# Performance work log

Hardware: AMD Instinct MI355X
Metric: run time of the kernel (lower is better)

The kernel has to match this reference:

```python
import jax, jax.numpy as jnp
import numpy as np

DFAUD = 1024
DFRGB = 1024
DIM_K = 1024
N_HEADS = 4
B, T = 16, 1024


def setup_inputs() -> dict:
    key = jax.random.key(0)
    ks = jax.random.split(key, 11)
    s = lambda d: 1.0 / np.sqrt(d)
    return {
        "x": jax.random.normal(ks[0], (B, T, DFAUD), jnp.float32),
        "y": jax.random.normal(ks[1], (B, T, DFRGB), jnp.float32),
        "adj": jax.random.normal(ks[2], (B, T, T), jnp.float32),
        "Wq": jax.random.uniform(ks[3], (DIM_K, DFAUD), jnp.float32, -s(DFAUD), s(DFAUD)),
        "bq": jnp.zeros((DIM_K,), jnp.float32),
        "Wk": jax.random.uniform(ks[4], (DIM_K, DFRGB), jnp.float32, -s(DFRGB), s(DFRGB)),
        "bk": jnp.zeros((DIM_K,), jnp.float32),
        "Wv": jax.random.uniform(ks[5], (DIM_K, DFRGB), jnp.float32, -s(DFRGB), s(DFRGB)),
        "bv": jnp.zeros((DIM_K,), jnp.float32),
        "Wo": jax.random.uniform(ks[6], (DFRGB, DIM_K), jnp.float32, -s(DIM_K), s(DIM_K)),
        "bo": jnp.zeros((DFRGB,), jnp.float32),
    }


def reference(x, y, adj, Wq, bq, Wk, bk, Wv, bv, Wo, bo):
    b, t = x.shape[0], x.shape[1]
    dh = DIM_K // N_HEADS
    norm = 1.0 / np.sqrt(DIM_K)
    # Faithful reproduction of the torch reshape(-1, B, T, dim_k // n_heads):
    # [B, T, dim_k] -> [n_heads, B, T, dh] (row-major reshape, layout-mixing for h>1)
    Q = (x @ Wq.T + bq).reshape(N_HEADS, b, t, dh)
    K = (y @ Wk.T + bk).reshape(N_HEADS, b, t, dh)
    V = (y @ Wv.T + bv).reshape(N_HEADS, b, t, dh)
    scores = jnp.einsum('hbqd,hbkd->hbqk', Q, K) * norm  # [h, B, T, T]
    att = jax.nn.softmax(scores + adj, axis=-1)          # adj [B,T,T] broadcasts
    temp = jnp.einsum('hbqk,hbkd->hbqd', att, V).reshape(b, t, DIM_K)
    out = (temp @ Wo.T + bo).reshape(-1, t, y.shape[2])
    return out
```

## Files before the change

### kernel.cpp

```cpp
#include <hip/hip_runtime.h>
#include <stdint.h>
#include <string.h>

typedef unsigned short u16;
typedef __attribute__((ext_vector_type(8))) short short8_t;
typedef __attribute__((ext_vector_type(4))) float f32x4;

typedef const __attribute__((address_space(1))) void GV;
typedef __attribute__((address_space(3))) void LV;

__device__ __forceinline__ void gload_lds16(const void* g, void* l) {
  __builtin_amdgcn_global_load_lds((GV*)g, (LV*)l, 16, 0, 0);
}

__device__ __forceinline__ u16 f2bf(float f) {
  union { float f; uint32_t u; } v; v.f = f;
  return (u16)((v.u + 0x7FFFu + ((v.u >> 16) & 1u)) >> 16);
}

__device__ __forceinline__ f32x4 fz4() { f32x4 v = {0.f, 0.f, 0.f, 0.f}; return v; }

__global__ __launch_bounds__(256) void cast2_kernel(const float* __restrict__ in0,
                                                    const float* __restrict__ in1,
                                                    u16* __restrict__ out0,
                                                    u16* __restrict__ out1) {
  const int half = blockIdx.x >> 14;
  const float* in = half ? in1 : in0;
  u16* out = half ? out1 : out0;
  int i = ((blockIdx.x & 16383) * 256 + threadIdx.x) * 4;
  float4 v = *(const float4*)(in + i);
  ushort4 o;
  o.x = f2bf(v.x); o.y = f2bf(v.y); o.z = f2bf(v.z); o.w = f2bf(v.w);
  *(ushort4*)(out + i) = o;
}

__global__ __launch_bounds__(256) void cast4_kernel(const float* __restrict__ w0,
                                                    const float* __restrict__ w1,
                                                    const float* __restrict__ w2,
                                                    const float* __restrict__ w3,
                                                    u16* __restrict__ o0,
                                                    u16* __restrict__ o1,
                                                    u16* __restrict__ o2,
                                                    u16* __restrict__ o3) {
  const int sel = blockIdx.x >> 10;
  const float* in = sel == 0 ? w0 : sel == 1 ? w1 : sel == 2 ? w2 : w3;
  u16* out = sel == 0 ? o0 : sel == 1 ? o1 : sel == 2 ? o2 : o3;
  int i = ((blockIdx.x & 1023) * 256 + threadIdx.x) * 4;
  float4 v = *(const float4*)(in + i);
  ushort4 o;
  o.x = f2bf(v.x); o.y = f2bf(v.y); o.z = f2bf(v.z); o.w = f2bf(v.w);
  *(ushort4*)(out + i) = o;
}

template <int OUT_BF16>
__global__ __launch_bounds__(512, 2) void gemm8(const u16* __restrict__ A,
                                                const u16* __restrict__ B,
                                                const float* __restrict__ bias,
                                                void* __restrict__ Cout,
                                                int M, int N, int K) {
  __shared__ u16 Al[2 * 16384];
  __shared__ u16 Bl[2 * 16384];
  const int tid = threadIdx.x, w = tid >> 6, l = tid & 63;
  const int g = l >> 4, q = l & 15;
  const int bid = blockIdx.x;
  const int xcd = bid & 7;
  const int nt = (bid >> 3) & 3;
  const int mt = xcd * 8 + (bid >> 5);
  const int n0 = nt * 256, m0 = mt * 256;
  const int wr = (w >> 2) * 128, wc = (w & 3) * 64;
  const int NT = K >> 6;
  const int ah = w >> 2;
  const int bh = (w & 3) >> 1;
  const int brow0 = ((w & 3) & 1) * 64;

#define STAGE_A(S, half)                                                          \
  {                                                                               \
    _Pragma("unroll") for (int j_ = 0; j_ < 2; ++j_) {                            \
      const int idx_ = j_ * 512 + tid;                                            \
      const int row_ = idx_ >> 3;                                                 \
      const int sl_ = (idx_ & 7) ^ (((idx_ >> 5) & 1) << 1);                      \
      gload_lds16(A + (size_t)(m0 + (half) * 128 + row_) * K + (S) * 64 + sl_ * 8,\
                  Al + ((S) & 1) * 16384 + (half) * 8192 + (j_ * 512 + w * 64) * 8);\
    }                                                                             \
  }
#define STAGE_B(S, half)                                                          \
  {                                                                               \
    _Pragma("unroll") for (int j_ = 0; j_ < 2; ++j_) {                            \
      const int idx_ = j_ * 512 + tid;                                            \
      const int row_ = idx_ >> 3;                                                 \
      const int sl_ = (idx_ & 7) ^ (((idx_ >> 5) & 1) << 1);                      \
      gload_lds16(B + (size_t)(n0 + (half) * 128 + row_) * K + (S) * 64 + sl_ * 8,\
                  Bl + ((S) & 1) * 16384 + (half) * 8192 + (j_ * 512 + w * 64) * 8);\
    }                                                                             \
  }

  f32x4 acc[8][4];
#pragma unroll
  for (int i = 0; i < 8; ++i)
#pragma unroll
    for (int n = 0; n < 4; ++n) acc[i][n] = fz4();

  float bv[4];
#pragma unroll
  for (int nf = 0; nf < 4; ++nf) bv[nf] = bias[n0 + wc + nf * 16 + q];

  STAGE_A(0, 0); STAGE_A(0, 1); STAGE_B(0, 0); STAGE_B(0, 1);
  STAGE_A(1, 0); STAGE_A(1, 1); STAGE_B(1, 0); STAGE_B(1, 1);
  asm volatile("s_waitcnt vmcnt(8)");
  __builtin_amdgcn_s_barrier();

  short8_t bfr[4][2];
  for (int S = 0; S < NT; ++S) {
    const int bs = (S & 1) * 16384;
#pragma unroll
    for (int p = 0; p < 4; ++p) {
      short8_t afr[2][2];
#pragma unroll
      for (int mi = 0; mi < 2; ++mi)
#pragma unroll
        for (int kk = 0; kk < 2; ++kk) {
          const int r = (2 * p + mi) * 16 + q;
          afr[mi][kk] = *(const short8_t*)(Al + bs + ah * 8192 + r * 64 +
                                           ((kk * 4 + g) ^ (((r >> 2) & 1) << 1)) * 8);
        }
      if (p == 0) {
#pragma unroll
        for (int nf = 0; nf < 4; ++nf)
#pragma unroll
          for (int kk = 0; kk < 2; ++kk) {
            const int r = brow0 + nf * 16 + q;
            bfr[nf][kk] = *(const short8_t*)(Bl + bs + bh * 8192 + r * 64 +
                                             ((kk * 4 + g) ^ (((r >> 2) & 1) << 1)) * 8);
          }
      }
      if (p == 0 && S >= 1 && S + 1 < NT) STAGE_A(S + 1, 0);
      if (p == 1 && S >= 1 && S + 1 < NT) STAGE_A(S + 1, 1);
      if (p == 2 && S + 2 < NT) STAGE_B(S + 2, 0);
      if (p == 3 && S + 2 < NT) STAGE_B(S + 2, 1);
      if (p == 3) {
        if (S == NT - 2) { asm volatile("s_waitcnt vmcnt(0)"); }
        else if (S < NT - 2) { asm volatile("s_waitcnt vmcnt(4)"); }
      }
      __builtin_amdgcn_s_barrier();
      asm volatile("s_waitcnt lgkmcnt(0)" ::: "memory");
      __builtin_amdgcn_sched_barrier(0);
      __builtin_amdgcn_s_setprio(1);
#pragma unroll
      for (int nf = 0; nf < 4; ++nf)
#pragma unroll
        for (int mi = 0; mi < 2; ++mi)
#pragma unroll
          for (int kk = 0; kk < 2; ++kk)
            acc[2 * p + mi][nf] = __builtin_amdgcn_mfma_f32_16x16x32_bf16(
                afr[mi][kk], bfr[nf][kk], acc[2 * p + mi][nf], 0, 0, 0);
      __builtin_amdgcn_s_setprio(0);
      __builtin_amdgcn_s_barrier();
    }
  }
#undef STAGE_A
#undef STAGE_B

#pragma unroll
  for (int nf = 0; nf < 4; ++nf) {
    const int col = n0 + wc + nf * 16 + q;
#pragma unroll
    for (int mf = 0; mf < 8; ++mf) {
      const int rowb = m0 + wr + mf * 16 + g * 4;
#pragma unroll
      for (int j = 0; j < 4; ++j) {
        const float vv = acc[mf][nf][j] + bv[nf];
        if (OUT_BF16)
          ((u16*)Cout)[(size_t)(rowb + j) * N + col] = f2bf(vv);
        else
          ((float*)Cout)[(size_t)(rowb + j) * N + col] = vv;
      }
    }
  }
}

__global__ __launch_bounds__(256) void transpose_v(const u16* __restrict__ V,
                                                   u16* __restrict__ VT) {
  __shared__ u16 t[64][68];
  const int hb = blockIdx.z;
  const int t0 = blockIdx.x * 64, d0 = blockIdx.y * 64;
  const u16* src = V + (size_t)hb * 1024 * 256;
  u16* dst = VT + (size_t)hb * 256 * 1024;
  const int tid = threadIdx.x;
#pragma unroll
  for (int i = 0; i < 4; ++i) {
    const int idx = i * 256 + tid;
    const int r = idx >> 4, c4 = (idx & 15) * 4;
    ushort4 v = *(const ushort4*)(src + (size_t)(t0 + r) * 256 + d0 + c4);
    *(ushort4*)&t[r][c4] = v;
  }
  __syncthreads();
#pragma unroll
  for (int i = 0; i < 4; ++i) {
    const int idx = i * 256 + tid;
    const int r = idx >> 4, c4 = (idx & 15) * 4;
    ushort4 v;
    v.x = t[c4][r]; v.y = t[c4 + 1][r]; v.z = t[c4 + 2][r]; v.w = t[c4 + 3][r];
    *(ushort4*)(dst + (size_t)(d0 + r) * 1024 + t0 + c4) = v;
  }
}

__global__ __launch_bounds__(256) void attn_kernel(const u16* __restrict__ Q,
                                                   const u16* __restrict__ Kf,
                                                   const u16* __restrict__ VT,
                                                   const float* __restrict__ adj,
                                                   u16* __restrict__ O) {
  __shared__ u16 Ks[32 * 256];
  __shared__ u16 Vs[256 * 32];
  const int tid = threadIdx.x, w = tid >> 6, l = tid & 63;
  const int g = l >> 4, q = l & 15;
  const int bid = blockIdx.x;
  const int xcd = bid & 7, idx = bid >> 3;
  const int b = xcd * 2 + (idx >> 6);
  const int qb = (idx >> 2) & 15, h = idx & 3;
  const int hb = h * 16 + b;
  const int q0 = qb * 64;
  const u16* qb_p = Q + ((size_t)hb * 1024 + q0 + w * 16) * 256;
  const u16* kb = Kf + (size_t)hb * 1024 * 256;
  const u16* vtb = VT + (size_t)hb * 256 * 1024;
  const float* adjr = adj + (size_t)b * 1024 * 1024 + (size_t)(q0 + w * 16 + q) * 1024;

  const int krow_b = tid >> 5;
  const int kslot = tid & 31;
  const int vdr_b = tid >> 2;
  const int vsl = tid & 3;

  short8_t qf[8];
#pragma unroll
  for (int kk = 0; kk < 8; ++kk)
    qf[kk] = *(const short8_t*)(qb_p + (size_t)q * 256 + kk * 32 + g * 8);

  f32x4 o[16];
#pragma unroll
  for (int n = 0; n < 16; ++n) o[n] = fz4();
  float mrun = -1e30f, lrun = 0.f;

  short8_t kst[4], vst[4];

#define LOADREGS(ktt)                                                              \
  {                                                                                \
    _Pragma("unroll") for (int i_ = 0; i_ < 4; ++i_) {                             \
      const int row_ = i_ * 8 + krow_b;                                            \
      kst[i_] = *(const short8_t*)(kb + (size_t)((ktt) * 32 + row_) * 256 +        \
                                   kslot * 8);                                     \
    }                                                                              \
    _Pragma("unroll") for (int i_ = 0; i_ < 4; ++i_) {                             \
      const int dr_ = i_ * 64 + vdr_b;                                             \
      vst[i_] = *(const short8_t*)(vtb + (size_t)dr_ * 1024 + (ktt) * 32 +         \
                                   vsl * 8);                                       \
    }                                                                              \
  }
#define WRITEREGS()                                                                \
  {                                                                                \
    _Pragma("unroll") for (int i_ = 0; i_ < 4; ++i_) {                             \
      const int row_ = i_ * 8 + krow_b;                                            \
      *(short8_t*)((char*)Ks + row_ * 512 + ((kslot ^ (row_ & 7)) * 16)) = kst[i_];\
    }                                                                              \
    _Pragma("unroll") for (int i_ = 0; i_ < 4; ++i_) {                             \
      const int dr_ = i_ * 64 + vdr_b;                                             \
      *(short8_t*)((char*)Vs + dr_ * 64 + ((vsl ^ ((dr_ >> 1) & 3)) * 16)) = vst[i_];\
    }                                                                              \
  }

  LOADREGS(0);
  float4 a0 = *(const float4*)(adjr + 0 * 32 + 0 * 16 + g * 4);
  float4 a1 = *(const float4*)(adjr + 0 * 32 + 1 * 16 + g * 4);
  WRITEREGS();
  __syncthreads();

  for (int kt = 0; kt < 32; ++kt) {
    float4 n0v = a0, n1v = a1;
    if (kt < 31) {
      LOADREGS(kt + 1);
      n0v = *(const float4*)(adjr + (kt + 1) * 32 + 0 * 16 + g * 4);
      n1v = *(const float4*)(adjr + (kt + 1) * 32 + 1 * 16 + g * 4);
    }

    f32x4 s[2];
    __builtin_amdgcn_s_setprio(1);
#pragma unroll
    for (int f = 0; f < 2; ++f) {
      f32x4 a = fz4();
      const int row = f * 16 + q;
      const char* kr = (const char*)Ks + row * 512;
#pragma unroll
      for (int kk = 0; kk < 8; ++kk) {
        const int cb = kk * 64 + g * 16;
        short8_t kfr = *(const short8_t*)(kr + (cb ^ ((row & 7) << 4)));
        a = __builtin_amdgcn_mfma_f32_16x16x32_bf16(kfr, qf[kk], a, 0, 0, 0);
      }
      s[f] = a;
    }
    __builtin_amdgcn_s_setprio(0);

#pragma unroll
    for (int j = 0; j < 4; ++j) {
      s[0][j] = s[0][j] * 0.03125f + ((const float*)&a0)[j];
      s[1][j] = s[1][j] * 0.03125f + ((const float*)&a1)[j];
    }

    float pmax = s[0][0];
#pragma unroll
    for (int j = 1; j < 4; ++j) pmax = fmaxf(pmax, s[0][j]);
#pragma unroll
    for (int j = 0; j < 4; ++j) pmax = fmaxf(pmax, s[1][j]);
    pmax = fmaxf(pmax, __shfl_xor(pmax, 16));
    pmax = fmaxf(pmax, __shfl_xor(pmax, 32));

    if (!__all(pmax - mrun <= 8.0f)) {
      const float mn = fmaxf(mrun, pmax);
      const float al = __expf(mrun - mn);
      mrun = mn;
      lrun *= al;
#pragma unroll
      for (int n = 0; n < 16; ++n)
#pragma unroll
        for (int r = 0; r < 4; ++r) o[n][r] *= al;
    }

    float sum = 0.f;
#pragma unroll
    for (int f = 0; f < 2; ++f)
#pragma unroll
      for (int j = 0; j < 4; ++j) {
        const float p = __expf(s[f][j] - mrun);
        s[f][j] = p;
        sum += p;
      }
    sum += __shfl_xor(sum, 16);
    sum += __shfl_xor(sum, 32);
    lrun += sum;

    uint32_t W00, W01, W10, W11;
    asm("v_cvt_pk_bf16_f32 %0, %1, %2" : "=v"(W00) : "v"(s[0][0]), "v"(s[0][1]));
    asm("v_cvt_pk_bf16_f32 %0, %1, %2" : "=v"(W01) : "v"(s[0][2]), "v"(s[0][3]));
    asm("v_cvt_pk_bf16_f32 %0, %1, %2" : "=v"(W10) : "v"(s[1][0]), "v"(s[1][1]));
    asm("v_cvt_pk_bf16_f32 %0, %1, %2" : "=v"(W11) : "v"(s[1][2]), "v"(s[1][3]));
    const uint32_t sA0 = (g < 2) ? W00 : W10;
    const uint32_t sA1 = (g < 2) ? W01 : W11;
    const uint32_t sB0 = (g < 2) ? W10 : W00;
    const uint32_t sB1 = (g < 2) ? W11 : W01;
    const uint32_t A0 = (uint32_t)__shfl_xor((int)sA0, 16);
    const uint32_t A1 = (uint32_t)__shfl_xor((int)sA1, 16);
    const uint32_t B0 = (uint32_t)__shfl_xor((int)sB0, 32);
    const uint32_t B1 = (uint32_t)__shfl_xor((int)sB1, 32);
    const uint32_t C0 = (uint32_t)__shfl_xor((int)sB0, 48);
    const uint32_t C1 = (uint32_t)__shfl_xor((int)sB1, 48);
    union { uint32_t u[4]; short8_t v; } pu;
    pu.u[0] = (g == 0) ? W00 : (g == 1) ? C0 : (g == 2) ? B0 : A0;
    pu.u[1] = (g == 0) ? W01 : (g == 1) ? C1 : (g == 2) ? B1 : A1;
    pu.u[2] = (g == 0) ? A0 : (g == 1) ? B0 : (g == 2) ? C0 : W10;
    pu.u[3] = (g == 0) ? A1 : (g == 1) ? B1 : (g == 2) ? C1 : W11;
    const short8_t pa = pu.v;

    __builtin_amdgcn_s_setprio(1);
#pragma unroll
    for (int n = 0; n < 16; ++n) {
      const int dr = n * 16 + q;
      const int sl = g ^ ((dr >> 1) & 3);
      short8_t vf = *(const short8_t*)((const char*)Vs + dr * 64 + sl * 16);
      o[n] = __builtin_amdgcn_mfma_f32_16x16x32_bf16(vf, pa, o[n], 0, 0, 0);
    }
    __builtin_amdgcn_s_setprio(0);

    if (kt < 31) {
      __syncthreads();
      WRITEREGS();
      __syncthreads();
    }
    a0 = n0v; a1 = n1v;
  }
#undef LOADREGS
#undef WRITEREGS

  const float inv = 1.0f / lrun;
  u16* ob = O + ((size_t)hb * 1024 + q0 + w * 16 + q) * 256;
#pragma unroll
  for (int n = 0; n < 16; ++n) {
    ushort4 st;
    st.x = f2bf(o[n][0] * inv); st.y = f2bf(o[n][1] * inv);
    st.z = f2bf(o[n][2] * inv); st.w = f2bf(o[n][3] * inv);
    *(ushort4*)(ob + n * 16 + g * 4) = st;
  }
}

extern "C" void kernel_launch(void* const* d_in, const int* in_sizes, int n_in,
                              void* d_out, int out_size, void* d_ws, size_t ws_size,
                              hipStream_t stream) {
  (void)in_sizes; (void)n_in; (void)out_size; (void)ws_size;
  const float* x   = (const float*)d_in[0];
  const float* y   = (const float*)d_in[1];
  const float* adj = (const float*)d_in[2];
  const float* Wq  = (const float*)d_in[3];
  const float* bq  = (const float*)d_in[4];
  const float* Wk  = (const float*)d_in[5];
  const float* bk  = (const float*)d_in[6];
  const float* Wv  = (const float*)d_in[7];
  const float* bv  = (const float*)d_in[8];
  const float* Wo  = (const float*)d_in[9];
  const float* bo  = (const float*)d_in[10];

  char* ws = (char*)d_ws;
  const size_t MB = 1ull << 20;
  u16* Xb  = (u16*)(ws + 0);
  u16* Yb  = (u16*)(ws + 32 * MB);
  u16* Wqb = (u16*)(ws + 64 * MB);
  u16* Wkb = (u16*)(ws + 66 * MB);
  u16* Wvb = (u16*)(ws + 68 * MB);
  u16* Wob = (u16*)(ws + 70 * MB);
  u16* Qb  = (u16*)(ws + 72 * MB);
  u16* Kb  = (u16*)(ws + 104 * MB);
  u16* Vb  = (u16*)(ws + 136 * MB);
  u16* VTb = (u16*)(ws + 168 * MB);
  u16* Tmp = Xb;

  cast2_kernel<<<32768, 256, 0, stream>>>(x, y, Xb, Yb);
  cast4_kernel<<<4096, 256, 0, stream>>>(Wq, Wk, Wv, Wo, Wqb, Wkb, Wvb, Wob);

  gemm8<1><<<256, 512, 0, stream>>>(Xb, Wqb, bq, Qb, 16384, 1024, 1024);
  gemm8<1><<<256, 512, 0, stream>>>(Yb, Wkb, bk, Kb, 16384, 1024, 1024);
  gemm8<1><<<256, 512, 0, stream>>>(Yb, Wvb, bv, Vb, 16384, 1024, 1024);

  transpose_v<<<dim3(16, 4, 64), 256, 0, stream>>>(Vb, VTb);

  attn_kernel<<<1024, 256, 0, stream>>>(Qb, Kb, VTb, adj, Tmp);

  gemm8<0><<<256, 512, 0, stream>>>(Tmp, Wob, bo, d_out, 16384, 1024, 1024);
}
```

Before: 356.5 us.

## Fuse QKV projections into one launch and write V pre-transposed from epilogue

Merges the three Q/K/V projection GEMMs into a single 768-block launch that selects operands by block index, and has the V GEMM epilogue write directly into the transposed per-head layout the attention kernel expects. This removes the separate transpose kernel, its extra read and write of V, and two launch gaps, while giving the GPU three times as many blocks to schedule. The transposed epilogue scatters 2-byte stores with a large stride, which may coalesce poorly.

```diff
diff --git a/kernel.cpp b/kernel.cpp
--- a/kernel.cpp
+++ b/kernel.cpp
@@ -52,22 +52,19 @@
   *(ushort4*)(out + i) = o;
 }
 
-template <int OUT_BF16>
-__global__ __launch_bounds__(512, 2) void gemm8(const u16* __restrict__ A,
-                                                const u16* __restrict__ B,
-                                                const float* __restrict__ bias,
-                                                void* __restrict__ Cout,
-                                                int M, int N, int K) {
-  __shared__ u16 Al[2 * 16384];
-  __shared__ u16 Bl[2 * 16384];
+__device__ __forceinline__ void gemm8_core(int bid, const u16* __restrict__ A,
+                                           const u16* __restrict__ B,
+                                           const float* __restrict__ bias,
+                                           void* __restrict__ Cout, int mode,
+                                           u16* Al, u16* Bl) {
+  const int M = 16384, N = 1024, K = 1024;
+  (void)M;
   const int tid = threadIdx.x, w = tid >> 6, l = tid & 63;
   const int g = l >> 4, q = l & 15;
-  const int bid = blockIdx.x;
   const int xcd = bid & 7;
   const int nt = (bid >> 3) & 3;
   const int mt = xcd * 8 + (bid >> 5);
   const int n0 = nt * 256, m0 = mt * 256;
-  const int wr = (w >> 2) * 128, wc = (w & 3) * 64;
   const int NT = K >> 6;
   const int ah = w >> 2;
   const int bh = (w & 3) >> 1;
@@ -102,7 +99,7 @@
 
   float bv[4];
 #pragma unroll
-  for (int nf = 0; nf < 4; ++nf) bv[nf] = bias[n0 + wc + nf * 16 + q];
+  for (int nf = 0; nf < 4; ++nf) bv[nf] = bias[n0 + (w & 3) * 64 + nf * 16 + q];
 
   STAGE_A(0, 0); STAGE_A(0, 1); STAGE_B(0, 0); STAGE_B(0, 1);
   STAGE_A(1, 0); STAGE_A(1, 1); STAGE_B(1, 0); STAGE_B(1, 1);
@@ -160,6 +157,7 @@
 #undef STAGE_A
 #undef STAGE_B
 
+  const int wr = (w >> 2) * 128, wc = (w & 3) * 64;
 #pragma unroll
   for (int nf = 0; nf < 4; ++nf) {
     const int col = n0 + wc + nf * 16 + q;
@@ -169,39 +167,52 @@
 #pragma unroll
       for (int j = 0; j < 4; ++j) {
         const float vv = acc[mf][nf][j] + bv[nf];
-        if (OUT_BF16)
-          ((u16*)Cout)[(size_t)(rowb + j) * N + col] = f2bf(vv);
-        else
-          ((float*)Cout)[(size_t)(rowb + j) * N + col] = vv;
+        const int row = rowb + j;
+        if (mode == 0) {
+          ((float*)Cout)[(size_t)row * N + col] = vv;
+        } else if (mode == 1) {
+          ((u16*)Cout)[(size_t)row * N + col] = f2bf(vv);
+        } else {
+          ((u16*)Cout)[((size_t)(row >> 8) << 18) + ((size_t)(col & 255) << 10) +
+                       ((row & 255) * 4) + (col >> 8)] = f2bf(vv);
+        }
       }
     }
   }
 }
 
-__global__ __launch_bounds__(256) void transpose_v(const u16* __restrict__ V,
-                                                   u16* __restrict__ VT) {
-  __shared__ u16 t[64][68];
-  const int hb = blockIdx.z;
-  const int t0 = blockIdx.x * 64, d0 = blockIdx.y * 64;
-  const u16* src = V + (size_t)hb * 1024 * 256;
-  u16* dst = VT + (size_t)hb * 256 * 1024;
-  const int tid = threadIdx.x;
-#pragma unroll
-  for (int i = 0; i < 4; ++i) {
-    const int idx = i * 256 + tid;
-    const int r = idx >> 4, c4 = (idx & 15) * 4;
-    ushort4 v = *(const ushort4*)(src + (size_t)(t0 + r) * 256 + d0 + c4);
-    *(ushort4*)&t[r][c4] = v;
-  }
-  __syncthreads();
-#pragma unroll
-  for (int i = 0; i < 4; ++i) {
-    const int idx = i * 256 + tid;
-    const int r = idx >> 4, c4 = (idx & 15) * 4;
-    ushort4 v;
-    v.x = t[c4][r]; v.y = t[c4 + 1][r]; v.z = t[c4 + 2][r]; v.w = t[c4 + 3][r];
-    *(ushort4*)(dst + (size_t)(d0 + r) * 1024 + t0 + c4) = v;
-  }
+__global__ __launch_bounds__(512, 2) void gemm8_qkv(const u16* __restrict__ Xb,
+                                                    const u16* __restrict__ Yb,
+                                                    const u16* __restrict__ Wqb,
+                                                    const u16* __restrict__ Wkb,
+                                                    const u16* __restrict__ Wvb,
+                                                    const float* __restrict__ bq,
+                                                    const float* __restrict__ bk,
+                                                    const float* __restrict__ bv,
+                                                    u16* __restrict__ Qb,
+                                                    u16* __restrict__ Kb,
+                                                    u16* __restrict__ VTb) {
+  __shared__ u16 Al[2 * 16384];
+  __shared__ u16 Bl[2 * 16384];
+  const int sel = blockIdx.x >> 8, bid = blockIdx.x & 255;
+  const u16* A;
+  const u16* B;
+  const float* bias;
+  void* C;
+  int mode;
+  if (sel == 0)      { A = Xb; B = Wqb; bias = bq; C = Qb;  mode = 1; }
+  else if (sel == 1) { A = Yb; B = Wkb; bias = bk; C = Kb;  mode = 1; }
+  else               { A = Yb; B = Wvb; bias = bv; C = VTb; mode = 2; }
+  gemm8_core(bid, A, B, bias, C, mode, Al, Bl);
+}
+
+__global__ __launch_bounds__(512, 2) void gemm8_out(const u16* __restrict__ A,
+                                                    const u16* __restrict__ B,
+                                                    const float* __restrict__ bias,
+                                                    float* __restrict__ C) {
+  __shared__ u16 Al[2 * 16384];
+  __shared__ u16 Bl[2 * 16384];
+  gemm8_core(blockIdx.x, A, B, bias, C, 0, Al, Bl);
 }
 
 __global__ __launch_bounds__(256) void attn_kernel(const u16* __restrict__ Q,
@@ -414,20 +425,15 @@
   u16* Wob = (u16*)(ws + 70 * MB);
   u16* Qb  = (u16*)(ws + 72 * MB);
   u16* Kb  = (u16*)(ws + 104 * MB);
-  u16* Vb  = (u16*)(ws + 136 * MB);
   u16* VTb = (u16*)(ws + 168 * MB);
   u16* Tmp = Xb;
 
   cast2_kernel<<<32768, 256, 0, stream>>>(x, y, Xb, Yb);
   cast4_kernel<<<4096, 256, 0, stream>>>(Wq, Wk, Wv, Wo, Wqb, Wkb, Wvb, Wob);
 
-  gemm8<1><<<256, 512, 0, stream>>>(Xb, Wqb, bq, Qb, 16384, 1024, 1024);
-  gemm8<1><<<256, 512, 0, stream>>>(Yb, Wkb, bk, Kb, 16384, 1024, 1024);
-  gemm8<1><<<256, 512, 0, stream>>>(Yb, Wvb, bv, Vb, 16384, 1024, 1024);
-
-  transpose_v<<<dim3(16, 4, 64), 256, 0, stream>>>(Vb, VTb);
+  gemm8_qkv<<<768, 512, 0, stream>>>(Xb, Yb, Wqb, Wkb, Wvb, bq, bk, bv, Qb, Kb, VTb);
 
   attn_kernel<<<1024, 256, 0, stream>>>(Qb, Kb, VTb, adj, Tmp);
 
-  gemm8<0><<<256, 512, 0, stream>>>(Tmp, Wob, bo, d_out, 16384, 1024, 1024);
-}
+  gemm8_out<<<256, 512, 0, stream>>>(Tmp, Wob, bo, (float*)d_out);
+}
```

After: 380.0 us. +6.6%, slower.

## Fuse V transpose into V projection GEMM epilogue with permuted B rows

Applied to the files above, without the earlier changes.

Adds a third GEMM mode that loads the V weight rows in a permuted order and writes its output straight into the transposed V layout the attention kernel expects. The separate transpose kernel and the intermediate V buffer go away, which removes one launch and a full 32MB read and write pass. The cost is a scattered epilogue store pattern, with 2-byte writes strided by 1024 elements, which may coalesce poorly.

```diff
diff --git a/kernel.cpp b/kernel.cpp
--- a/kernel.cpp
+++ b/kernel.cpp
@@ -52,7 +52,7 @@
   *(ushort4*)(out + i) = o;
 }
 
-template <int OUT_BF16>
+template <int MODE>
 __global__ __launch_bounds__(512, 2) void gemm8(const u16* __restrict__ A,
                                                 const u16* __restrict__ B,
                                                 const float* __restrict__ bias,
@@ -67,11 +67,12 @@
   const int nt = (bid >> 3) & 3;
   const int mt = xcd * 8 + (bid >> 5);
   const int n0 = nt * 256, m0 = mt * 256;
-  const int wr = (w >> 2) * 128, wc = (w & 3) * 64;
   const int NT = K >> 6;
   const int ah = w >> 2;
   const int bh = (w & 3) >> 1;
   const int brow0 = ((w & 3) & 1) * 64;
+
+#define BROW(u) (MODE == 2 ? ((((u) >> 6) << 8) + nt * 64 + ((u) & 63)) : (n0 + (u)))
 
 #define STAGE_A(S, half)                                                          \
   {                                                                               \
@@ -89,7 +90,8 @@
       const int idx_ = j_ * 512 + tid;                                            \
       const int row_ = idx_ >> 3;                                                 \
       const int sl_ = (idx_ & 7) ^ (((idx_ >> 5) & 1) << 1);                      \
-      gload_lds16(B + (size_t)(n0 + (half) * 128 + row_) * K + (S) * 64 + sl_ * 8,\
+      const int pr_ = BROW((half) * 128 + row_);                                  \
+      gload_lds16(B + (size_t)pr_ * K + (S) * 64 + sl_ * 8,                       \
                   Bl + ((S) & 1) * 16384 + (half) * 8192 + (j_ * 512 + w * 64) * 8);\
     }                                                                             \
   }
@@ -100,9 +102,10 @@
 #pragma unroll
     for (int n = 0; n < 4; ++n) acc[i][n] = fz4();
 
+  const int wc = (w & 3) * 64;
   float bv[4];
 #pragma unroll
-  for (int nf = 0; nf < 4; ++nf) bv[nf] = bias[n0 + wc + nf * 16 + q];
+  for (int nf = 0; nf < 4; ++nf) bv[nf] = bias[BROW(wc + nf * 16 + q)];
 
   STAGE_A(0, 0); STAGE_A(0, 1); STAGE_B(0, 0); STAGE_B(0, 1);
   STAGE_A(1, 0); STAGE_A(1, 1); STAGE_B(1, 0); STAGE_B(1, 1);
@@ -160,48 +163,31 @@
 #undef STAGE_A
 #undef STAGE_B
 
+  const int wr = (w >> 2) * 128;
+  const int s4 = wc >> 6;
 #pragma unroll
   for (int nf = 0; nf < 4; ++nf) {
     const int col = n0 + wc + nf * 16 + q;
+    const int dvt = nt * 64 + nf * 16 + q;
 #pragma unroll
     for (int mf = 0; mf < 8; ++mf) {
       const int rowb = m0 + wr + mf * 16 + g * 4;
 #pragma unroll
       for (int j = 0; j < 4; ++j) {
         const float vv = acc[mf][nf][j] + bv[nf];
-        if (OUT_BF16)
-          ((u16*)Cout)[(size_t)(rowb + j) * N + col] = f2bf(vv);
-        else
-          ((float*)Cout)[(size_t)(rowb + j) * N + col] = vv;
+        const int row = rowb + j;
+        if (MODE == 0) {
+          ((float*)Cout)[(size_t)row * N + col] = vv;
+        } else if (MODE == 1) {
+          ((u16*)Cout)[(size_t)row * N + col] = f2bf(vv);
+        } else {
+          ((u16*)Cout)[((size_t)(row >> 8) << 18) + ((size_t)dvt << 10) +
+                       ((row & 255) * 4) + s4] = f2bf(vv);
+        }
       }
     }
   }
-}
-
-__global__ __launch_bounds__(256) void transpose_v(const u16* __restrict__ V,
-                                                   u16* __restrict__ VT) {
-  __shared__ u16 t[64][68];
-  const int hb = blockIdx.z;
-  const int t0 = blockIdx.x * 64, d0 = blockIdx.y * 64;
-  const u16* src = V + (size_t)hb * 1024 * 256;
-  u16* dst = VT + (size_t)hb * 256 * 1024;
-  const int tid = threadIdx.x;
-#pragma unroll
-  for (int i = 0; i < 4; ++i) {
-    const int idx = i * 256 + tid;
-    const int r = idx >> 4, c4 = (idx & 15) * 4;
-    ushort4 v = *(const ushort4*)(src + (size_t)(t0 + r) * 256 + d0 + c4);
-    *(ushort4*)&t[r][c4] = v;
-  }
-  __syncthreads();
-#pragma unroll
-  for (int i = 0; i < 4; ++i) {
-    const int idx = i * 256 + tid;
-    const int r = idx >> 4, c4 = (idx & 15) * 4;
-    ushort4 v;
-    v.x = t[c4][r]; v.y = t[c4 + 1][r]; v.z = t[c4 + 2][r]; v.w = t[c4 + 3][r];
-    *(ushort4*)(dst + (size_t)(d0 + r) * 1024 + t0 + c4) = v;
-  }
+#undef BROW
 }
 
 __global__ __launch_bounds__(256) void attn_kernel(const u16* __restrict__ Q,
@@ -414,7 +400,6 @@
   u16* Wob = (u16*)(ws + 70 * MB);
   u16* Qb  = (u16*)(ws + 72 * MB);
   u16* Kb  = (u16*)(ws + 104 * MB);
-  u16* Vb  = (u16*)(ws + 136 * MB);
   u16* VTb = (u16*)(ws + 168 * MB);
   u16* Tmp = Xb;
 
@@ -423,9 +408,7 @@
 
   gemm8<1><<<256, 512, 0, stream>>>(Xb, Wqb, bq, Qb, 16384, 1024, 1024);
   gemm8<1><<<256, 512, 0, stream>>>(Yb, Wkb, bk, Kb, 16384, 1024, 1024);
-  gemm8<1><<<256, 512, 0, stream>>>(Yb, Wvb, bv, Vb, 16384, 1024, 1024);
-
-  transpose_v<<<dim3(16, 4, 64), 256, 0, stream>>>(Vb, VTb);
+  gemm8<2><<<256, 512, 0, stream>>>(Yb, Wvb, bv, VTb, 16384, 1024, 1024);
 
   attn_kernel<<<1024, 256, 0, stream>>>(Qb, Kb, VTb, adj, Tmp);
 
```

New measurement: 360.1 us. No clear change (+1.0%).
